# Kernel optimization log

Measured on AMD Instinct MI355X. Metric: run time of the kernel, lower is better.

The kernel has to match this reference:

```python
import jax, jax.numpy as jnp
from jax import lax
import numpy as np

H_SIZE = 1024      # max(hidden_size_list)
EXPAND = 2
INTER = EXPAND * H_SIZE            # 2048 intermediate size
NHEADS = 32                        # max(num_heads_list)
HEAD_DIM = INTER // NHEADS         # 64
NSTATE = 128                       # ssm state size
NGROUPS = 1
KCONV = 4                          # conv kernel
CHUNK = 256                        # chunk size for SSD scan
EPS = 1e-5                         # layer_norm_epsilon
CONV_DIM = INTER + 2 * NGROUPS * NSTATE        # 2304
PROJ_DIM = 2 * INTER + 2 * NGROUPS * NSTATE + NHEADS  # 4352


def setup_inputs() -> dict:
    key = jax.random.key(0)
    ks = jax.random.split(key, 9)
    B, S = 2, 4096
    return {
        "hidden_states": jax.random.normal(ks[0], (B, S, H_SIZE), jnp.float32),
        "in_proj_w": jax.random.normal(ks[1], (PROJ_DIM, H_SIZE), jnp.float32) * 0.02,
        "conv_w": jax.random.normal(ks[2], (CONV_DIM, 1, KCONV), jnp.float32) * 0.2,
        "conv_b": jax.random.normal(ks[3], (CONV_DIM,), jnp.float32) * 0.02,
        "dt_bias": jax.random.normal(ks[4], (NHEADS,), jnp.float32) * 0.1,
        "A_log": jax.random.uniform(ks[5], (NHEADS,), jnp.float32, 0.0, 1.0),
        "D": jax.random.normal(ks[6], (NHEADS,), jnp.float32),
        "norm_w": jnp.ones((INTER,), jnp.float32) + 0.01 * jax.random.normal(ks[7], (INTER,), jnp.float32),
        "out_proj_w": jax.random.normal(ks[8], (H_SIZE, INTER), jnp.float32) * 0.02,
    }


def _segsum(a):
    # a: [B,H,C,L] -> lower-triangular segment sums [B,H,C,L,L]
    L = a.shape[-1]
    cs = jnp.cumsum(a, axis=-1)
    ss = cs[..., :, None] - cs[..., None, :]
    mask = jnp.tril(jnp.ones((L, L), dtype=bool))
    return jnp.where(mask, ss, -jnp.inf)


def reference(hidden_states, in_proj_w, conv_w, conv_b, dt_bias, A_log, D, norm_w, out_proj_w):
    B, S, _ = hidden_states.shape
    proj = hidden_states @ in_proj_w.T                       # [B,S,4352]
    gate = proj[..., :INTER]                                 # [B,S,2048]
    hBC = proj[..., INTER:INTER + CONV_DIM]                  # [B,S,2304]
    dt = proj[..., INTER + CONV_DIM:]                        # [B,S,H]

    # causal depthwise conv1d + SiLU
    xc_ = jnp.transpose(hBC, (0, 2, 1))                      # [B,C,S]
    xc_ = lax.conv_general_dilated(xc_, conv_w, (1,), [(KCONV - 1, 0)],
                                   dimension_numbers=('NCH', 'OIH', 'NCH'),
                                   feature_group_count=CONV_DIM)
    xc_ = jax.nn.silu(xc_ + conv_b[None, :, None])
    hBC = jnp.transpose(xc_, (0, 2, 1))                      # [B,S,2304]

    h = hBC[..., :INTER]
    Bm = hBC[..., INTER:INTER + NGROUPS * NSTATE]
    Cm = hBC[..., INTER + NGROUPS * NSTATE:]

    dt = jax.nn.softplus(dt + dt_bias)                       # [B,S,H]
    dt = jnp.clip(dt, 0.0, None)                             # time_step_limit (0, inf)
    A = -jnp.exp(A_log)                                      # [H]

    NC = S // CHUNK
    xh = h.reshape(B, NC, CHUNK, NHEADS, HEAD_DIM)
    Bh = jnp.repeat(Bm.reshape(B, NC, CHUNK, NGROUPS, NSTATE), NHEADS // NGROUPS, axis=3)
    Ch = jnp.repeat(Cm.reshape(B, NC, CHUNK, NGROUPS, NSTATE), NHEADS // NGROUPS, axis=3)
    dtc = dt.reshape(B, NC, CHUNK, NHEADS)

    a = jnp.transpose(dtc * A, (0, 3, 1, 2))                 # [B,H,NC,L]
    A_cum = jnp.cumsum(a, axis=-1)                           # [B,H,NC,L]
    Lmat = jnp.exp(_segsum(a))                               # [B,H,NC,L,L]
    xdt = xh * dtc[..., None]                                # [B,NC,L,H,P]

    # intra-chunk (diagonal block) output
    Yd = jnp.einsum('bclhn,bcshn,bhcls,bcshp->bclhp', Ch, Bh, Lmat, xdt)

    # per-chunk final states
    decay = jnp.exp(A_cum[..., -1:] - A_cum)                 # [B,H,NC,L]
    states = jnp.einsum('bclhn,bhcl,bclhp->bchpn', Bh, decay, xdt)  # [B,NC,H,P,N]

    # inter-chunk recurrence over chunks
    g = jnp.exp(A_cum[..., -1])                              # [B,H,NC]
    def step(carry, inp):
        s_c, g_c = inp
        return carry * g_c[..., None, None] + s_c, carry
    _, prev = lax.scan(step, jnp.zeros((B, NHEADS, HEAD_DIM, NSTATE), states.dtype),
                       (jnp.moveaxis(states, 1, 0), jnp.moveaxis(g, 2, 0)))
    prev = jnp.moveaxis(prev, 0, 1)                          # [B,NC,H,P,N] state entering each chunk

    Yo = jnp.einsum('bclhn,bchpn,bhcl->bclhp', Ch, prev, jnp.exp(A_cum))

    y = (Yd + Yo + D[None, None, None, :, None] * xh).reshape(B, S, INTER)

    # gated RMSNorm (fp32 internally)
    yf = y.astype(jnp.float32) * jax.nn.silu(gate.astype(jnp.float32))
    var = jnp.mean(yf * yf, axis=-1, keepdims=True)
    y = norm_w * (yf * lax.rsqrt(var + EPS))

    return y @ out_proj_w.T
```

## Files before the change

kernel.cpp:

```cpp
#include <hip/hip_runtime.h>
#include <hip/hip_bf16.h>
#include <math.h>

#define H_SIZE   1024
#define INTER    2048
#define NHEADS   32
#define HEAD_DIM 64
#define NSTATE   128
#define KCONV    4
#define CHUNK    256
#define CONV_DIM (INTER + 2*NSTATE)
#define CIN_DIM  (CONV_DIM + NHEADS)
#define PROJ_DIM (2*INTER + 2*NSTATE + NHEADS)
#define BATCH    2
#define SEQ      4096
#define NC       (SEQ/CHUNK)
#define EPS_F    1e-5f

typedef __attribute__((ext_vector_type(8))) short bf16x8;
typedef __attribute__((ext_vector_type(4))) float f32x4;
typedef unsigned short ushort_t;

__device__ __forceinline__ ushort_t f2bf(float x) {
  unsigned u = __float_as_uint(x);
  u += 0x7fffu + ((u >> 16) & 1u);
  return (ushort_t)(u >> 16);
}
__device__ __forceinline__ float bf2f(ushort_t h) {
  return __uint_as_float((unsigned)h << 16);
}

__global__ __launch_bounds__(256) void convert_hl_kernel(
    const float* __restrict__ x, ushort_t* __restrict__ hi,
    ushort_t* __restrict__ lo, int n4) {
  int idx = blockIdx.x * 256 + threadIdx.x;
  int stride = gridDim.x * 256;
  for (int i = idx; i < n4; i += stride) {
    const float* p = x + (size_t)i * 4;
    float v0 = p[0], v1 = p[1], v2 = p[2], v3 = p[3];
    ushort_t h0 = f2bf(v0), h1 = f2bf(v1), h2 = f2bf(v2), h3 = f2bf(v3);
    ushort_t l0 = f2bf(v0 - bf2f(h0));
    ushort_t l1 = f2bf(v1 - bf2f(h1));
    ushort_t l2 = f2bf(v2 - bf2f(h2));
    ushort_t l3 = f2bf(v3 - bf2f(h3));
    *(uint2*)(hi + (size_t)i * 4) =
        make_uint2((unsigned)h0 | ((unsigned)h1 << 16), (unsigned)h2 | ((unsigned)h3 << 16));
    *(uint2*)(lo + (size_t)i * 4) =
        make_uint2((unsigned)l0 | ((unsigned)l1 << 16), (unsigned)l2 | ((unsigned)l3 << 16));
  }
}

#define LROW 40
template<int PLANES>
__global__ __launch_bounds__(256) void gemm_hl_mfma_kernel(
    const ushort_t* __restrict__ Ahi, const ushort_t* __restrict__ Alo,
    const ushort_t* __restrict__ Whi, const ushort_t* __restrict__ Wlo,
    float* __restrict__ C, int M, int N, int K, int nx, int ldc) {
  __shared__ __align__(16) ushort_t Ah[128*LROW];
  __shared__ __align__(16) ushort_t Al[(PLANES==3) ? 128*LROW : 8];
  __shared__ __align__(16) ushort_t Wh[128*LROW], Wl[128*LROW];
  const int tid = threadIdx.x;
  const int lane = tid & 63, wid = tid >> 6;
  const int wr = wid >> 1, wc = wid & 1;
  const int fr = lane & 15, fg = lane >> 4;

  const int cpx = gridDim.x >> 3;
  const int logical = (blockIdx.x & 7) * cpx + (blockIdx.x >> 3);
  const int grp = logical / (nx * 4);
  const int rem = logical - grp * (nx * 4);
  const int bx = rem >> 2;
  const int by = grp * 4 + (rem & 3);
  const int m0 = by * 128, n0 = bx * 128;

  const int r0 = tid >> 2;
  const int kseg = (tid & 3) * 8;
  const int r1 = r0 + 64;
  const size_t a0 = (size_t)(m0 + r0) * K + kseg;
  const size_t a1 = (size_t)(m0 + r1) * K + kseg;
  const size_t w0 = (size_t)(n0 + r0) * K + kseg;
  const size_t w1 = (size_t)(n0 + r1) * K + kseg;
  const bool wv0 = (n0 + r0) < N, wv1 = (n0 + r1) < N;

  bf16x8 gA0, gA1, gAl0, gAl1, gW0, gW1, gWl0, gWl1;
  const bf16x8 z8 = {};
  f32x4 acc[4][4] = {};

  auto glod = [&](int k0) {
    gA0  = *(const bf16x8*)(Ahi + a0 + k0);
    gA1  = *(const bf16x8*)(Ahi + a1 + k0);
    if constexpr (PLANES == 3) {
      gAl0 = *(const bf16x8*)(Alo + a0 + k0);
      gAl1 = *(const bf16x8*)(Alo + a1 + k0);
    }
    gW0  = wv0 ? *(const bf16x8*)(Whi + w0 + k0) : z8;
    gW1  = wv1 ? *(const bf16x8*)(Whi + w1 + k0) : z8;
    gWl0 = wv0 ? *(const bf16x8*)(Wlo + w0 + k0) : z8;
    gWl1 = wv1 ? *(const bf16x8*)(Wlo + w1 + k0) : z8;
  };

  glod(0);
  for (int k0 = 0; k0 < K; k0 += 32) {
    __syncthreads();
    *(bf16x8*)&Ah[r0*LROW + kseg] = gA0;
    *(bf16x8*)&Ah[r1*LROW + kseg] = gA1;
    if constexpr (PLANES == 3) {
      *(bf16x8*)&Al[r0*LROW + kseg] = gAl0;
      *(bf16x8*)&Al[r1*LROW + kseg] = gAl1;
    }
    *(bf16x8*)&Wh[r0*LROW + kseg] = gW0;
    *(bf16x8*)&Wh[r1*LROW + kseg] = gW1;
    *(bf16x8*)&Wl[r0*LROW + kseg] = gWl0;
    *(bf16x8*)&Wl[r1*LROW + kseg] = gWl1;
    __syncthreads();
    if (k0 + 32 < K) glod(k0 + 32);

    bf16x8 wh[4], wl[4];
#pragma unroll
    for (int nf = 0; nf < 4; ++nf) {
      int off = (wc*64 + nf*16 + fr) * LROW + 8*fg;
      wh[nf] = *(const bf16x8*)&Wh[off];
      wl[nf] = *(const bf16x8*)&Wl[off];
    }
#pragma unroll
    for (int mf = 0; mf < 4; ++mf) {
      int aoff = (wr*64 + mf*16 + fr) * LROW + 8*fg;
      bf16x8 ah = *(const bf16x8*)&Ah[aoff];
      bf16x8 al;
      if constexpr (PLANES == 3) al = *(const bf16x8*)&Al[aoff];
#pragma unroll
      for (int nf = 0; nf < 4; ++nf) {
        acc[mf][nf] = __builtin_amdgcn_mfma_f32_16x16x32_bf16(ah, wh[nf], acc[mf][nf], 0, 0, 0);
        acc[mf][nf] = __builtin_amdgcn_mfma_f32_16x16x32_bf16(ah, wl[nf], acc[mf][nf], 0, 0, 0);
        if constexpr (PLANES == 3)
          acc[mf][nf] = __builtin_amdgcn_mfma_f32_16x16x32_bf16(al, wh[nf], acc[mf][nf], 0, 0, 0);
      }
    }
  }

#pragma unroll
  for (int mf = 0; mf < 4; ++mf)
#pragma unroll
    for (int nf = 0; nf < 4; ++nf) {
      int col = n0 + wc*64 + nf*16 + fr;
      if (col < N) {
        size_t base = (size_t)(m0 + wr*64 + mf*16 + fg*4) * ldc + col;
        f32x4 v = acc[mf][nf];
        C[base]                 = v[0];
        C[base + (size_t)ldc]   = v[1];
        C[base + 2*(size_t)ldc] = v[2];
        C[base + 3*(size_t)ldc] = v[3];
      }
    }
}

__global__ __launch_bounds__(256) void conv2_kernel(
    const float* __restrict__ cin, const float* __restrict__ cw,
    const float* __restrict__ cb, float* __restrict__ hbc,
    ushort_t* __restrict__ Bph, ushort_t* __restrict__ Bpl,
    ushort_t* __restrict__ Cph, ushort_t* __restrict__ Cpl) {
  const int c = blockIdx.x * 256 + threadIdx.x;
  const int r0 = blockIdx.y * 8;
  const int s0 = r0 & (SEQ - 1);
  const float w0 = cw[c*KCONV+0], w1 = cw[c*KCONV+1];
  const float w2 = cw[c*KCONV+2], w3 = cw[c*KCONV+3];
  const float bias = cb[c];
  const float* cp = cin + (size_t)r0 * CIN_DIM + c;
  float xm3 = (s0 > 0) ? cp[-3*CIN_DIM] : 0.f;
  float xm2 = (s0 > 0) ? cp[-2*CIN_DIM] : 0.f;
  float xm1 = (s0 > 0) ? cp[-1*CIN_DIM] : 0.f;
#pragma unroll
  for (int i = 0; i < 8; ++i) {
    float x0 = cp[(size_t)i * CIN_DIM];
    float acc = fmaf(w0, xm3, fmaf(w1, xm2, fmaf(w2, xm1, fmaf(w3, x0, bias))));
    acc = acc / (1.f + expf(-acc));
    size_t row = (size_t)(r0 + i);
    if (c < INTER) {
      hbc[row*CONV_DIM + c] = acc;
    } else {
      ushort_t hh = f2bf(acc);
      ushort_t ll = f2bf(acc - bf2f(hh));
      int cc = c - INTER;
      if (cc < NSTATE) { Bph[row*NSTATE + cc] = hh; Bpl[row*NSTATE + cc] = ll; }
      else { Cph[row*NSTATE + (cc-NSTATE)] = hh; Cpl[row*NSTATE + (cc-NSTATE)] = ll; }
    }
    xm3 = xm2; xm2 = xm1; xm1 = x0;
  }
}

__global__ __launch_bounds__(256) void cumsum_kernel(
    const float* __restrict__ cin, const float* __restrict__ A_log,
    const float* __restrict__ dtb, float* __restrict__ dtp,
    float* __restrict__ acum, float* __restrict__ gch) {
  const int c = blockIdx.x, h = blockIdx.y, b = blockIdx.z;
  const int tid = threadIdx.x;
  __shared__ float sm[CHUNK];
  const float A = -expf(A_log[h]);
  const int s = c * CHUNK + tid;
  const size_t row = (size_t)(b*SEQ + s);
  float draw = cin[row*CIN_DIM + CONV_DIM + h] + dtb[h];
  float d = (draw > 20.f) ? draw : log1pf(expf(draw));
  dtp[row*NHEADS + h] = d;
  float a = d * A;
  sm[tid] = a;
  __syncthreads();
  for (int off = 1; off < CHUNK; off <<= 1) {
    float v = 0.f;
    if (tid >= off) v = sm[tid - off];
    __syncthreads();
    sm[tid] += v;
    __syncthreads();
  }
  float ac = sm[tid];
  acum[((size_t)(b*NHEADS + h)*NC + c)*CHUNK + tid] = ac;
  if (tid == CHUNK-1) gch[(size_t)(b*NHEADS + h)*NC + c] = expf(ac);
}

#define CBROW 136
#define XROW2 72
__global__ __launch_bounds__(256) void yd_mfma_kernel(
    const ushort_t* __restrict__ Bph, const ushort_t* __restrict__ Bpl,
    const ushort_t* __restrict__ Cph, const ushort_t* __restrict__ Cpl,
    const float* __restrict__ hbc, const float* __restrict__ acum,
    const float* __restrict__ dtp, const float* __restrict__ Dv,
    float* __restrict__ y) {
  __shared__ __align__(16) ushort_t BhS[64*CBROW], BlS[64*CBROW];
  __shared__ __align__(16) ushort_t XhS[64*XROW2], XlS[64*XROW2];
  __shared__ __align__(16) ushort_t GhS[4][16*XROW2], GlS[4][16*XROW2];
  __shared__ float acLs[64], acSs[64];

  const int h = blockIdx.x;
  const int c = blockIdx.y >> 2, lt = blockIdx.y & 3;
  const int b = blockIdx.z;
  const int tid = threadIdx.x;
  const int lane = tid & 63, w = tid >> 6;
  const int fr = lane & 15, fg = lane >> 4;

  const size_t seqbase = (size_t)(b*SEQ + c*CHUNK);
  const size_t acbase  = ((size_t)(b*NHEADS + h)*NC + c)*CHUNK;

  bf16x8 cfh[4], cfl[4];
  {
    const size_t cg = (seqbase + lt*64 + w*16 + fr) * 128;
#pragma unroll
    for (int ks = 0; ks < 4; ++ks) {
      int ko = ks*32 + fg*8;
      cfh[ks] = *(const bf16x8*)(Cph + cg + ko);
      cfl[ks] = *(const bf16x8*)(Cpl + cg + ko);
    }
  }
  if (tid < 64) acLs[tid] = acum[acbase + lt*64 + tid];

  f32x4 acc[4] = {};

  for (int st = 0; st <= lt; ++st) {
    __syncthreads();
    {
      const size_t g0 = (seqbase + st*64) * 128;
#pragma unroll
      for (int i = 0; i < 4; ++i) {
        int f = tid + 256*i; int r = f >> 4; int k8 = (f & 15) * 8;
        *(bf16x8*)&BhS[r*CBROW + k8] = *(const bf16x8*)(Bph + g0 + (size_t)r*128 + k8);
        *(bf16x8*)&BlS[r*CBROW + k8] = *(const bf16x8*)(Bpl + g0 + (size_t)r*128 + k8);
      }
    }
#pragma unroll
    for (int i = 0; i < 4; ++i) {
      int f = tid + 256*i; int s = f >> 4; int p0 = (f & 15) * 4;
      size_t row = seqbase + st*64 + s;
      float dtv = dtp[row*NHEADS + h];
      float4 xv = *(const float4*)(hbc + row*CONV_DIM + h*HEAD_DIM + p0);
      float vals[4] = {xv.x*dtv, xv.y*dtv, xv.z*dtv, xv.w*dtv};
#pragma unroll
      for (int j = 0; j < 4; ++j) {
        int p = p0 + j;
        int sw = s ^ (((p >> 2) & 7) << 3);
        ushort_t hh = f2bf(vals[j]);
        ushort_t ll = f2bf(vals[j] - bf2f(hh));
        XhS[p*XROW2 + sw] = hh;
        XlS[p*XROW2 + sw] = ll;
      }
    }
    if (tid < 64) acSs[tid] = acum[acbase + st*64 + tid];
    __syncthreads();

    f32x4 g[4] = {};
#pragma unroll
    for (int ks = 0; ks < 4; ++ks) {
      const int ko = ks*32 + fg*8;
#pragma unroll
      for (int nf = 0; nf < 4; ++nf) {
        const int rb = (nf*16 + fr) * CBROW + ko;
        bf16x8 bh = *(const bf16x8*)&BhS[rb];
        bf16x8 bl = *(const bf16x8*)&BlS[rb];
        g[nf] = __builtin_amdgcn_mfma_f32_16x16x32_bf16(cfh[ks], bh, g[nf], 0, 0, 0);
        g[nf] = __builtin_amdgcn_mfma_f32_16x16x32_bf16(cfh[ks], bl, g[nf], 0, 0, 0);
        g[nf] = __builtin_amdgcn_mfma_f32_16x16x32_bf16(cfl[ks], bh, g[nf], 0, 0, 0);
      }
    }
    {
      const bool full = (st < lt);
#pragma unroll
      for (int nf = 0; nf < 4; ++nf) {
        int sl = nf*16 + fr;
        float aS = acSs[sl];
#pragma unroll
        for (int r = 0; r < 4; ++r) {
          int ll = w*16 + fg*4 + r;
          float v = 0.f;
          if (full || ll >= sl) v = g[nf][r] * __expf(acLs[ll] - aS);
          ushort_t hh = f2bf(v);
          ushort_t lo2 = f2bf(v - bf2f(hh));
          GhS[w][(fg*4 + r)*XROW2 + sl] = hh;
          GlS[w][(fg*4 + r)*XROW2 + sl] = lo2;
        }
      }
    }
    __syncthreads();
#pragma unroll
    for (int ks = 0; ks < 2; ++ks) {
      const int ko = ks*32 + fg*8;
      bf16x8 gh = *(const bf16x8*)&GhS[w][fr*XROW2 + ko];
      bf16x8 gl = *(const bf16x8*)&GlS[w][fr*XROW2 + ko];
#pragma unroll
      for (int nf = 0; nf < 4; ++nf) {
        int p = nf*16 + fr;
        int kb = ko ^ (((p >> 2) & 7) << 3);
        bf16x8 xh = *(const bf16x8*)&XhS[p*XROW2 + kb];
        bf16x8 xl = *(const bf16x8*)&XlS[p*XROW2 + kb];
        acc[nf] = __builtin_amdgcn_mfma_f32_16x16x32_bf16(gh, xh, acc[nf], 0, 0, 0);
        acc[nf] = __builtin_amdgcn_mfma_f32_16x16x32_bf16(gh, xl, acc[nf], 0, 0, 0);
        acc[nf] = __builtin_amdgcn_mfma_f32_16x16x32_bf16(gl, xh, acc[nf], 0, 0, 0);
      }
    }
  }

  const float Dh = Dv[h];
#pragma unroll
  for (int nf = 0; nf < 4; ++nf) {
    int p = nf*16 + fr;
#pragma unroll
    for (int r = 0; r < 4; ++r) {
      size_t row = seqbase + lt*64 + w*16 + fg*4 + r;
      float xval = hbc[row*CONV_DIM + h*HEAD_DIM + p];
      y[row*INTER + h*HEAD_DIM + p] = acc[nf][r] + Dh * xval;
    }
  }
}

#define SXROW 72
__global__ __launch_bounds__(256) void states_mfma_kernel(
    const ushort_t* __restrict__ Bph, const ushort_t* __restrict__ Bpl,
    const float* __restrict__ hbc, const float* __restrict__ acum,
    const float* __restrict__ dtp, float* __restrict__ states) {
  __shared__ __align__(16) ushort_t XhS[64*SXROW], XlS[64*SXROW];
  __shared__ __align__(16) ushort_t BhS[128*SXROW], BlS[128*SXROW];
  const int h = blockIdx.x, c = blockIdx.y, b = blockIdx.z;
  const int tid = threadIdx.x;
  const int lane = tid & 63, w = tid >> 6;
  const int fr = lane & 15, fg = lane >> 4;
  const size_t seqbase = (size_t)(b*SEQ + c*CHUNK);
  const size_t acbase  = ((size_t)(b*NHEADS + h)*NC + c)*CHUNK;
  const float aclast = acum[acbase + CHUNK - 1];
  f32x4 acc[8] = {};

  for (int lt = 0; lt < 4; ++lt) {
    __syncthreads();
#pragma unroll
    for (int i = 0; i < 4; ++i) {
      int f = tid + 256*i; int l = f >> 4; int p0 = (f & 15) * 4;
      size_t row = seqbase + lt*64 + l;
      float mult = dtp[row*NHEADS + h] * __expf(aclast - acum[acbase + lt*64 + l]);
      float4 xv = *(const float4*)(hbc + row*CONV_DIM + h*HEAD_DIM + p0);
      float vals[4] = {xv.x*mult, xv.y*mult, xv.z*mult, xv.w*mult};
#pragma unroll
      for (int j = 0; j < 4; ++j) {
        int p = p0 + j;
        int sw = l ^ (((p >> 2) & 7) << 3);
        ushort_t hh = f2bf(vals[j]);
        XhS[p*SXROW + sw] = hh;
        XlS[p*SXROW + sw] = f2bf(vals[j] - bf2f(hh));
      }
    }
#pragma unroll
    for (int i = 0; i < 4; ++i) {
      int f = tid + 256*i; int l = f >> 4; int n8 = (f & 15) * 8;
      size_t g0 = (seqbase + lt*64 + l) * 128 + n8;
      bf16x8 bh = *(const bf16x8*)(Bph + g0);
      bf16x8 bl = *(const bf16x8*)(Bpl + g0);
#pragma unroll
      for (int j = 0; j < 8; ++j) {
        int n = n8 + j;
        int sw = l ^ (((n >> 2) & 7) << 3);
        BhS[n*SXROW + sw] = (ushort_t)bh[j];
        BlS[n*SXROW + sw] = (ushort_t)bl[j];
      }
    }
    __syncthreads();
#pragma unroll
    for (int ks = 0; ks < 2; ++ks) {
      const int ko = ks*32 + fg*8;
      const int pa = w*16 + fr;
      const int ka = ko ^ (((pa >> 2) & 7) << 3);
      bf16x8 ah = *(const bf16x8*)&XhS[pa*SXROW + ka];
      bf16x8 al = *(const bf16x8*)&XlS[pa*SXROW + ka];
#pragma unroll
      for (int nf = 0; nf < 8; ++nf) {
        const int nb = nf*16 + fr;
        const int kb = ko ^ (((nb >> 2) & 7) << 3);
        bf16x8 bh = *(const bf16x8*)&BhS[nb*SXROW + kb];
        bf16x8 bl = *(const bf16x8*)&BlS[nb*SXROW + kb];
        acc[nf] = __builtin_amdgcn_mfma_f32_16x16x32_bf16(ah, bh, acc[nf], 0, 0, 0);
        acc[nf] = __builtin_amdgcn_mfma_f32_16x16x32_bf16(ah, bl, acc[nf], 0, 0, 0);
        acc[nf] = __builtin_amdgcn_mfma_f32_16x16x32_bf16(al, bh, acc[nf], 0, 0, 0);
      }
    }
  }
  float* sp = states + ((size_t)(b*NC + c)*NHEADS + h)*HEAD_DIM*NSTATE;
#pragma unroll
  for (int nf = 0; nf < 8; ++nf) {
    int n = nf*16 + fr;
#pragma unroll
    for (int r = 0; r < 4; ++r) {
      int p = w*16 + fg*4 + r;
      sp[(size_t)p*NSTATE + n] = acc[nf][r];
    }
  }
}

__global__ __launch_bounds__(1024) void scan_kernel(
    float* __restrict__ st, const float* __restrict__ g) {
  const int bh = blockIdx.x;
  const int b = bh >> 5, h = bh & 31;
  const int tid = threadIdx.x;
  float carry[8];
#pragma unroll
  for (int i = 0; i < 8; ++i) carry[i] = 0.f;
  for (int c = 0; c < NC; ++c) {
    const float gc = g[(size_t)(b*NHEADS + h)*NC + c];
    float* base = st + ((size_t)(b*NC + c)*NHEADS + h)*HEAD_DIM*NSTATE;
    ushort_t* ub = (ushort_t*)base;
    float sv[8];
#pragma unroll
    for (int i = 0; i < 8; ++i) sv[i] = base[i*1024 + tid];
    __syncthreads();
#pragma unroll
    for (int i = 0; i < 8; ++i) {
      int e = i*1024 + tid;
      ushort_t hh = f2bf(carry[i]);
      ub[e]        = hh;
      ub[8192 + e] = f2bf(carry[i] - bf2f(hh));
      carry[i] = fmaf(carry[i], gc, sv[i]);
    }
  }
}

#define PROW 136
__global__ __launch_bounds__(256) void yo_mfma_kernel(
    const ushort_t* __restrict__ Cph, const ushort_t* __restrict__ Cpl,
    const ushort_t* __restrict__ stp, const float* __restrict__ acum,
    float* __restrict__ y) {
  __shared__ __align__(16) ushort_t PhS[64*PROW], PlS[64*PROW];
  const int h = blockIdx.x, c = blockIdx.y, b = blockIdx.z;
  const int tid = threadIdx.x;
  const int lane = tid & 63, w = tid >> 6;
  const int fr = lane & 15, fg = lane >> 4;
  const size_t seqbase = (size_t)(b*SEQ + c*CHUNK);
  const size_t acbase  = ((size_t)(b*NHEADS + h)*NC + c)*CHUNK;

  const ushort_t* pb = stp + ((size_t)(b*NC + c)*NHEADS + h) * (size_t)(2*HEAD_DIM*NSTATE);
#pragma unroll
  for (int i = 0; i < 4; ++i) {
    int f = tid + 256*i; int r = f >> 4; int k8 = (f & 15) * 8;
    *(bf16x8*)&PhS[r*PROW + k8] = *(const bf16x8*)(pb + (size_t)r*128 + k8);
    *(bf16x8*)&PlS[r*PROW + k8] = *(const bf16x8*)(pb + 8192 + (size_t)r*128 + k8);
  }
  __syncthreads();

  for (int lt = 0; lt < 4; ++lt) {
    const size_t cg = (seqbase + lt*64 + w*16 + fr) * 128;
    f32x4 acc[4] = {};
#pragma unroll
    for (int ks = 0; ks < 4; ++ks) {
      int ko = ks*32 + fg*8;
      bf16x8 ah = *(const bf16x8*)(Cph + cg + ko);
      bf16x8 al = *(const bf16x8*)(Cpl + cg + ko);
#pragma unroll
      for (int nf = 0; nf < 4; ++nf) {
        const int rb = (nf*16 + fr) * PROW + ko;
        bf16x8 bh = *(const bf16x8*)&PhS[rb];
        bf16x8 bl = *(const bf16x8*)&PlS[rb];
        acc[nf] = __builtin_amdgcn_mfma_f32_16x16x32_bf16(ah, bh, acc[nf], 0, 0, 0);
        acc[nf] = __builtin_amdgcn_mfma_f32_16x16x32_bf16(ah, bl, acc[nf], 0, 0, 0);
        acc[nf] = __builtin_amdgcn_mfma_f32_16x16x32_bf16(al, bh, acc[nf], 0, 0, 0);
      }
    }
#pragma unroll
    for (int r = 0; r < 4; ++r) {
      int lrow = lt*64 + w*16 + fg*4 + r;
      float e = __expf(acum[acbase + lrow]);
      float* yrow = y + (seqbase + lrow)*INTER + h*HEAD_DIM;
#pragma unroll
      for (int nf = 0; nf < 4; ++nf) {
        int p = nf*16 + fr;
        yrow[p] += e * acc[nf][r];
      }
    }
  }
}

__global__ __launch_bounds__(256) void rms_kernel(
    const float* __restrict__ y, const float* __restrict__ gate,
    const float* __restrict__ norm_w, ushort_t* __restrict__ yh) {
  const int bs = blockIdx.x;
  const int tid = threadIdx.x;
  const float* yrow = y + (size_t)bs * INTER;
  const float* grow = gate + (size_t)bs * INTER;
  float yf[8];
  float ss = 0.f;
#pragma unroll
  for (int i = 0; i < 8; ++i) {
    int c = tid + i*256;
    float v = yrow[c];
    float gt = grow[c];
    float f = v * (gt / (1.f + expf(-gt)));
    yf[i] = f;
    ss += f*f;
  }
#pragma unroll
  for (int off = 32; off >= 1; off >>= 1) ss += __shfl_xor(ss, off, 64);
  __shared__ float red[4];
  if ((tid & 63) == 0) red[tid >> 6] = ss;
  __syncthreads();
  float total = red[0] + red[1] + red[2] + red[3];
  float sc = rsqrtf(total * (1.f/INTER) + EPS_F);
#pragma unroll
  for (int i = 0; i < 8; ++i) {
    int c = tid + i*256;
    yh[(size_t)bs*INTER + c] = f2bf(norm_w[c] * yf[i] * sc);
  }
}

__global__ void zero_kernel(float* p, size_t n) {
  size_t i = (size_t)blockIdx.x * blockDim.x + threadIdx.x;
  if (i < n) p[i] = 0.f;
}

extern "C" void kernel_launch(void* const* d_in, const int* in_sizes, int n_in,
                              void* d_out, int out_size, void* d_ws, size_t ws_size,
                              hipStream_t stream) {
  const float* hidden = (const float*)d_in[0];
  const float* in_w   = (const float*)d_in[1];
  const float* conv_w = (const float*)d_in[2];
  const float* conv_b = (const float*)d_in[3];
  const float* dt_b   = (const float*)d_in[4];
  const float* A_log  = (const float*)d_in[5];
  const float* Dv     = (const float*)d_in[6];
  const float* norm_w = (const float*)d_in[7];
  const float* out_w  = (const float*)d_in[8];
  float* out = (float*)d_out;

  const int M = BATCH*SEQ;

  const size_t sz_cin  = (size_t)M * CIN_DIM;
  const size_t sz_hbc  = (size_t)M * CONV_DIM;
  const size_t sz_dtp  = (size_t)M * NHEADS;
  const size_t sz_acum = (size_t)BATCH*NHEADS*NC*CHUNK;
  const size_t sz_gch  = (size_t)BATCH*NHEADS*NC;
  const size_t sz_R    = (size_t)BATCH*NC*NHEADS*HEAD_DIM*NSTATE;
  const size_t need = (sz_cin + sz_hbc + sz_dtp + sz_acum + sz_gch + sz_R) * sizeof(float);

  if (ws_size < need) {
    size_t n = (size_t)out_size;
    zero_kernel<<<(unsigned)((n + 255) / 256), 256, 0, stream>>>(out, n);
    return;
  }

  float* ws = (float*)d_ws;
  size_t o = 0;
  float* cin  = ws + o; o += sz_cin;
  float* hbc  = ws + o; o += sz_hbc;
  float* dtp  = ws + o; o += sz_dtp;
  float* acum = ws + o; o += sz_acum;
  float* gch  = ws + o; o += sz_gch;
  float* R    = ws + o; o += sz_R;

  float* y    = cin;
  float* gate = hbc;
  float* st   = R;

  ushort_t* hidhi = (ushort_t*)R;
  ushort_t* hidlo = hidhi + (size_t)M * H_SIZE;
  ushort_t* yhR   = (ushort_t*)R;
  ushort_t* wplh  = (ushort_t*)hbc;

  ushort_t* wscr = (ushort_t*)out;
  const size_t MP = (size_t)M * 128;
  ushort_t* bcp  = (ushort_t*)((char*)d_out + (size_t)(16u << 20));
  ushort_t* Bph = bcp;
  ushort_t* Bpl = bcp + MP;
  ushort_t* Cph = bcp + 2*MP;
  ushort_t* Cpl = bcp + 3*MP;

  {
    int nA4 = (M * H_SIZE) / 4;
    int nW  = CIN_DIM * H_SIZE;
    convert_hl_kernel<<<2048, 256, 0, stream>>>(hidden, hidhi, hidlo, nA4);
    convert_hl_kernel<<<2048, 256, 0, stream>>>(in_w + (size_t)INTER*H_SIZE, wscr, wscr + nW, nW/4);
    gemm_hl_mfma_kernel<2><<<16 * (M/128), 256, 0, stream>>>(
        hidhi, hidlo, wscr, wscr + nW, cin, M, 2048, H_SIZE, 16, CIN_DIM);
    gemm_hl_mfma_kernel<3><<<3 * (M/128), 256, 0, stream>>>(
        hidhi, hidlo, wscr + (size_t)2048*H_SIZE, wscr + nW + (size_t)2048*H_SIZE,
        cin + 2048, M, 288, H_SIZE, 3, CIN_DIM);
  }
  conv2_kernel<<<dim3(CONV_DIM/256, M/8), 256, 0, stream>>>(
      cin, conv_w, conv_b, hbc, Bph, Bpl, Cph, Cpl);
  cumsum_kernel<<<dim3(NC, NHEADS, BATCH), 256, 0, stream>>>(
      cin, A_log, dt_b, dtp, acum, gch);
  yd_mfma_kernel<<<dim3(NHEADS, NC*4, BATCH), 256, 0, stream>>>(
      Bph, Bpl, Cph, Cpl, hbc, acum, dtp, Dv, y);
  states_mfma_kernel<<<dim3(NHEADS, NC, BATCH), 256, 0, stream>>>(
      Bph, Bpl, hbc, acum, dtp, st);
  scan_kernel<<<dim3(BATCH*NHEADS), 1024, 0, stream>>>(st, gch);
  yo_mfma_kernel<<<dim3(NHEADS, NC, BATCH), 256, 0, stream>>>(
      Cph, Cpl, (const ushort_t*)st, acum, y);
  {
    int nA4 = (M * H_SIZE) / 4;
    int nW  = INTER * H_SIZE;
    convert_hl_kernel<<<2048, 256, 0, stream>>>(hidden, hidhi, hidlo, nA4);
    convert_hl_kernel<<<2048, 256, 0, stream>>>(in_w, wscr, wscr + nW, nW/4);
    gemm_hl_mfma_kernel<2><<<16 * (M/128), 256, 0, stream>>>(
        hidhi, hidlo, wscr, wscr + nW, gate, M, INTER, H_SIZE, 16, INTER);
  }
  rms_kernel<<<dim3(M), 256, 0, stream>>>(y, gate, norm_w, yhR);
  {
    int nW  = H_SIZE * INTER;
    convert_hl_kernel<<<2048, 256, 0, stream>>>(out_w, wplh, wplh + nW, nW/4);
    gemm_hl_mfma_kernel<2><<<8 * (M/128), 256, 0, stream>>>(
        yhR, yhR, wplh, wplh + nW, out, M, H_SIZE, INTER, 8, H_SIZE);
  }
}
```

Baseline: 659.6 us.

## Store conv output transposed as bf16 hi/lo pairs, read directly in MFMA kernels

```diff
diff --git a/kernel.cpp b/kernel.cpp
--- a/kernel.cpp
+++ b/kernel.cpp
@@ -11,9 +11,9 @@
 #define CHUNK    256
 #define CONV_DIM (INTER + 2*NSTATE)
 #define CIN_DIM  (CONV_DIM + NHEADS)
-#define PROJ_DIM (2*INTER + 2*NSTATE + NHEADS)
 #define BATCH    2
 #define SEQ      4096
+#define MT       (BATCH*SEQ)
 #define NC       (SEQ/CHUNK)
 #define EPS_F    1e-5f
 
@@ -155,11 +155,12 @@
 
 __global__ __launch_bounds__(256) void conv2_kernel(
     const float* __restrict__ cin, const float* __restrict__ cw,
-    const float* __restrict__ cb, float* __restrict__ hbc,
-    ushort_t* __restrict__ Bph, ushort_t* __restrict__ Bpl,
-    ushort_t* __restrict__ Cph, ushort_t* __restrict__ Cpl) {
+    const float* __restrict__ cb, ushort_t* __restrict__ xTh,
+    ushort_t* __restrict__ xTl, ushort_t* __restrict__ Bph,
+    ushort_t* __restrict__ Bpl, ushort_t* __restrict__ Cph,
+    ushort_t* __restrict__ Cpl) {
   const int c = blockIdx.x * 256 + threadIdx.x;
-  const int r0 = blockIdx.y * 8;
+  const int r0 = blockIdx.y * 32;
   const int s0 = r0 & (SEQ - 1);
   const float w0 = cw[c*KCONV+0], w1 = cw[c*KCONV+1];
   const float w2 = cw[c*KCONV+2], w3 = cw[c*KCONV+3];
@@ -168,22 +169,42 @@
   float xm3 = (s0 > 0) ? cp[-3*CIN_DIM] : 0.f;
   float xm2 = (s0 > 0) ? cp[-2*CIN_DIM] : 0.f;
   float xm1 = (s0 > 0) ? cp[-1*CIN_DIM] : 0.f;
-#pragma unroll
-  for (int i = 0; i < 8; ++i) {
-    float x0 = cp[(size_t)i * CIN_DIM];
-    float acc = fmaf(w0, xm3, fmaf(w1, xm2, fmaf(w2, xm1, fmaf(w3, x0, bias))));
-    acc = acc / (1.f + expf(-acc));
-    size_t row = (size_t)(r0 + i);
-    if (c < INTER) {
-      hbc[row*CONV_DIM + c] = acc;
-    } else {
+
+  if (c < INTER) {
+    ushort_t hb[32], lb[32];
+#pragma unroll
+    for (int i = 0; i < 32; ++i) {
+      float x0 = cp[(size_t)i * CIN_DIM];
+      float acc = fmaf(w0, xm3, fmaf(w1, xm2, fmaf(w2, xm1, fmaf(w3, x0, bias))));
+      acc = acc / (1.f + expf(-acc));
+      ushort_t hh = f2bf(acc);
+      hb[i] = hh; lb[i] = f2bf(acc - bf2f(hh));
+      xm3 = xm2; xm2 = xm1; xm1 = x0;
+    }
+    ushort_t* ph = xTh + (size_t)c * MT + r0;
+    ushort_t* pl = xTl + (size_t)c * MT + r0;
+#pragma unroll
+    for (int j = 0; j < 4; ++j) {
+      bf16x8 vh, vl;
+#pragma unroll
+      for (int k = 0; k < 8; ++k) { vh[k] = (short)hb[j*8+k]; vl[k] = (short)lb[j*8+k]; }
+      *(bf16x8*)(ph + j*8) = vh;
+      *(bf16x8*)(pl + j*8) = vl;
+    }
+  } else {
+    const int cc = c - INTER;
+#pragma unroll
+    for (int i = 0; i < 32; ++i) {
+      float x0 = cp[(size_t)i * CIN_DIM];
+      float acc = fmaf(w0, xm3, fmaf(w1, xm2, fmaf(w2, xm1, fmaf(w3, x0, bias))));
+      acc = acc / (1.f + expf(-acc));
+      size_t row = (size_t)(r0 + i);
       ushort_t hh = f2bf(acc);
       ushort_t ll = f2bf(acc - bf2f(hh));
-      int cc = c - INTER;
       if (cc < NSTATE) { Bph[row*NSTATE + cc] = hh; Bpl[row*NSTATE + cc] = ll; }
       else { Cph[row*NSTATE + (cc-NSTATE)] = hh; Cpl[row*NSTATE + (cc-NSTATE)] = ll; }
-    }
-    xm3 = xm2; xm2 = xm1; xm1 = x0;
+      xm3 = xm2; xm2 = xm1; xm1 = x0;
+    }
   }
 }
 
@@ -216,17 +237,16 @@
 }
 
 #define CBROW 136
-#define XROW2 72
+#define GROW  72
 __global__ __launch_bounds__(256) void yd_mfma_kernel(
     const ushort_t* __restrict__ Bph, const ushort_t* __restrict__ Bpl,
     const ushort_t* __restrict__ Cph, const ushort_t* __restrict__ Cpl,
-    const float* __restrict__ hbc, const float* __restrict__ acum,
-    const float* __restrict__ dtp, const float* __restrict__ Dv,
-    float* __restrict__ y) {
+    const ushort_t* __restrict__ xTh, const ushort_t* __restrict__ xTl,
+    const float* __restrict__ acum, const float* __restrict__ dtp,
+    const float* __restrict__ Dv, float* __restrict__ y) {
   __shared__ __align__(16) ushort_t BhS[64*CBROW], BlS[64*CBROW];
-  __shared__ __align__(16) ushort_t XhS[64*XROW2], XlS[64*XROW2];
-  __shared__ __align__(16) ushort_t GhS[4][16*XROW2], GlS[4][16*XROW2];
-  __shared__ float acLs[64], acSs[64];
+  __shared__ __align__(16) ushort_t GhS[4][16*GROW], GlS[4][16*GROW];
+  __shared__ float acLs[64], acSs[64], dtSs[64];
 
   const int h = blockIdx.x;
   const int c = blockIdx.y >> 2, lt = blockIdx.y & 3;
@@ -263,24 +283,8 @@
         *(bf16x8*)&BlS[r*CBROW + k8] = *(const bf16x8*)(Bpl + g0 + (size_t)r*128 + k8);
       }
     }
-#pragma unroll
-    for (int i = 0; i < 4; ++i) {
-      int f = tid + 256*i; int s = f >> 4; int p0 = (f & 15) * 4;
-      size_t row = seqbase + st*64 + s;
-      float dtv = dtp[row*NHEADS + h];
-      float4 xv = *(const float4*)(hbc + row*CONV_DIM + h*HEAD_DIM + p0);
-      float vals[4] = {xv.x*dtv, xv.y*dtv, xv.z*dtv, xv.w*dtv};
-#pragma unroll
-      for (int j = 0; j < 4; ++j) {
-        int p = p0 + j;
-        int sw = s ^ (((p >> 2) & 7) << 3);
-        ushort_t hh = f2bf(vals[j]);
-        ushort_t ll = f2bf(vals[j] - bf2f(hh));
-        XhS[p*XROW2 + sw] = hh;
-        XlS[p*XROW2 + sw] = ll;
-      }
-    }
     if (tid < 64) acSs[tid] = acum[acbase + st*64 + tid];
+    else if (tid < 128) dtSs[tid-64] = dtp[(seqbase + st*64 + (tid-64))*NHEADS + h];
     __syncthreads();
 
     f32x4 g[4] = {};
@@ -303,15 +307,16 @@
       for (int nf = 0; nf < 4; ++nf) {
         int sl = nf*16 + fr;
         float aS = acSs[sl];
+        float dS = dtSs[sl];
 #pragma unroll
         for (int r = 0; r < 4; ++r) {
           int ll = w*16 + fg*4 + r;
           float v = 0.f;
-          if (full || ll >= sl) v = g[nf][r] * __expf(acLs[ll] - aS);
+          if (full || ll >= sl) v = g[nf][r] * __expf(acLs[ll] - aS) * dS;
           ushort_t hh = f2bf(v);
           ushort_t lo2 = f2bf(v - bf2f(hh));
-          GhS[w][(fg*4 + r)*XROW2 + sl] = hh;
-          GlS[w][(fg*4 + r)*XROW2 + sl] = lo2;
+          GhS[w][(fg*4 + r)*GROW + sl] = hh;
+          GlS[w][(fg*4 + r)*GROW + sl] = lo2;
         }
       }
     }
@@ -319,14 +324,13 @@
 #pragma unroll
     for (int ks = 0; ks < 2; ++ks) {
       const int ko = ks*32 + fg*8;
-      bf16x8 gh = *(const bf16x8*)&GhS[w][fr*XROW2 + ko];
-      bf16x8 gl = *(const bf16x8*)&GlS[w][fr*XROW2 + ko];
+      bf16x8 gh = *(const bf16x8*)&GhS[w][fr*GROW + ko];
+      bf16x8 gl = *(const bf16x8*)&GlS[w][fr*GROW + ko];
 #pragma unroll
       for (int nf = 0; nf < 4; ++nf) {
-        int p = nf*16 + fr;
-        int kb = ko ^ (((p >> 2) & 7) << 3);
-        bf16x8 xh = *(const bf16x8*)&XhS[p*XROW2 + kb];
-        bf16x8 xl = *(const bf16x8*)&XlS[p*XROW2 + kb];
+        const size_t xb = (size_t)(h*HEAD_DIM + nf*16 + fr) * MT + seqbase + st*64 + ko;
+        bf16x8 xh = *(const bf16x8*)(xTh + xb);
+        bf16x8 xl = *(const bf16x8*)(xTl + xb);
         acc[nf] = __builtin_amdgcn_mfma_f32_16x16x32_bf16(gh, xh, acc[nf], 0, 0, 0);
         acc[nf] = __builtin_amdgcn_mfma_f32_16x16x32_bf16(gh, xl, acc[nf], 0, 0, 0);
         acc[nf] = __builtin_amdgcn_mfma_f32_16x16x32_bf16(gl, xh, acc[nf], 0, 0, 0);
@@ -338,10 +342,11 @@
 #pragma unroll
   for (int nf = 0; nf < 4; ++nf) {
     int p = nf*16 + fr;
+    const size_t xrow0 = (size_t)(h*HEAD_DIM + p) * MT + seqbase + lt*64 + w*16 + fg*4;
 #pragma unroll
     for (int r = 0; r < 4; ++r) {
       size_t row = seqbase + lt*64 + w*16 + fg*4 + r;
-      float xval = hbc[row*CONV_DIM + h*HEAD_DIM + p];
+      float xval = bf2f(xTh[xrow0 + r]) + bf2f(xTl[xrow0 + r]);
       y[row*INTER + h*HEAD_DIM + p] = acc[nf][r] + Dh * xval;
     }
   }
@@ -350,9 +355,9 @@
 #define SXROW 72
 __global__ __launch_bounds__(256) void states_mfma_kernel(
     const ushort_t* __restrict__ Bph, const ushort_t* __restrict__ Bpl,
-    const float* __restrict__ hbc, const float* __restrict__ acum,
-    const float* __restrict__ dtp, float* __restrict__ states) {
-  __shared__ __align__(16) ushort_t XhS[64*SXROW], XlS[64*SXROW];
+    const ushort_t* __restrict__ xTh, const ushort_t* __restrict__ xTl,
+    const float* __restrict__ acum, const float* __restrict__ dtp,
+    float* __restrict__ states) {
   __shared__ __align__(16) ushort_t BhS[128*SXROW], BlS[128*SXROW];
   const int h = blockIdx.x, c = blockIdx.y, b = blockIdx.z;
   const int tid = threadIdx.x;
@@ -367,42 +372,29 @@
     __syncthreads();
 #pragma unroll
     for (int i = 0; i < 4; ++i) {
-      int f = tid + 256*i; int l = f >> 4; int p0 = (f & 15) * 4;
+      int f = tid + 256*i; int l = f >> 4; int n8 = (f & 15) * 8;
       size_t row = seqbase + lt*64 + l;
       float mult = dtp[row*NHEADS + h] * __expf(aclast - acum[acbase + lt*64 + l]);
-      float4 xv = *(const float4*)(hbc + row*CONV_DIM + h*HEAD_DIM + p0);
-      float vals[4] = {xv.x*mult, xv.y*mult, xv.z*mult, xv.w*mult};
-#pragma unroll
-      for (int j = 0; j < 4; ++j) {
-        int p = p0 + j;
-        int sw = l ^ (((p >> 2) & 7) << 3);
-        ushort_t hh = f2bf(vals[j]);
-        XhS[p*SXROW + sw] = hh;
-        XlS[p*SXROW + sw] = f2bf(vals[j] - bf2f(hh));
-      }
-    }
-#pragma unroll
-    for (int i = 0; i < 4; ++i) {
-      int f = tid + 256*i; int l = f >> 4; int n8 = (f & 15) * 8;
-      size_t g0 = (seqbase + lt*64 + l) * 128 + n8;
+      size_t g0 = row * 128 + n8;
       bf16x8 bh = *(const bf16x8*)(Bph + g0);
       bf16x8 bl = *(const bf16x8*)(Bpl + g0);
 #pragma unroll
       for (int j = 0; j < 8; ++j) {
         int n = n8 + j;
         int sw = l ^ (((n >> 2) & 7) << 3);
-        BhS[n*SXROW + sw] = (ushort_t)bh[j];
-        BlS[n*SXROW + sw] = (ushort_t)bl[j];
+        float bv = (bf2f((ushort_t)bh[j]) + bf2f((ushort_t)bl[j])) * mult;
+        ushort_t hh = f2bf(bv);
+        BhS[n*SXROW + sw] = hh;
+        BlS[n*SXROW + sw] = f2bf(bv - bf2f(hh));
       }
     }
     __syncthreads();
 #pragma unroll
     for (int ks = 0; ks < 2; ++ks) {
       const int ko = ks*32 + fg*8;
-      const int pa = w*16 + fr;
-      const int ka = ko ^ (((pa >> 2) & 7) << 3);
-      bf16x8 ah = *(const bf16x8*)&XhS[pa*SXROW + ka];
-      bf16x8 al = *(const bf16x8*)&XlS[pa*SXROW + ka];
+      const size_t xb = (size_t)(h*HEAD_DIM + w*16 + fr) * MT + seqbase + lt*64 + ko;
+      bf16x8 ah = *(const bf16x8*)(xTh + xb);
+      bf16x8 al = *(const bf16x8*)(xTl + xb);
 #pragma unroll
       for (int nf = 0; nf < 8; ++nf) {
         const int nb = nf*16 + fr;
@@ -559,7 +551,7 @@
   const float* out_w  = (const float*)d_in[8];
   float* out = (float*)d_out;
 
-  const int M = BATCH*SEQ;
+  const int M = MT;
 
   const size_t sz_cin  = (size_t)M * CIN_DIM;
   const size_t sz_hbc  = (size_t)M * CONV_DIM;
@@ -587,6 +579,9 @@
   float* y    = cin;
   float* gate = hbc;
   float* st   = R;
+
+  ushort_t* xTh = (ushort_t*)hbc;
+  ushort_t* xTl = xTh + (size_t)INTER * MT;
 
   ushort_t* hidhi = (ushort_t*)R;
   ushort_t* hidlo = hidhi + (size_t)M * H_SIZE;
@@ -612,14 +607,14 @@
         hidhi, hidlo, wscr + (size_t)2048*H_SIZE, wscr + nW + (size_t)2048*H_SIZE,
         cin + 2048, M, 288, H_SIZE, 3, CIN_DIM);
   }
-  conv2_kernel<<<dim3(CONV_DIM/256, M/8), 256, 0, stream>>>(
-      cin, conv_w, conv_b, hbc, Bph, Bpl, Cph, Cpl);
+  conv2_kernel<<<dim3(CONV_DIM/256, M/32), 256, 0, stream>>>(
+      cin, conv_w, conv_b, xTh, xTl, Bph, Bpl, Cph, Cpl);
   cumsum_kernel<<<dim3(NC, NHEADS, BATCH), 256, 0, stream>>>(
       cin, A_log, dt_b, dtp, acum, gch);
   yd_mfma_kernel<<<dim3(NHEADS, NC*4, BATCH), 256, 0, stream>>>(
-      Bph, Bpl, Cph, Cpl, hbc, acum, dtp, Dv, y);
+      Bph, Bpl, Cph, Cpl, xTh, xTl, acum, dtp, Dv, y);
   states_mfma_kernel<<<dim3(NHEADS, NC, BATCH), 256, 0, stream>>>(
-      Bph, Bpl, hbc, acum, dtp, st);
+      Bph, Bpl, xTh, xTl, acum, dtp, st);
   scan_kernel<<<dim3(BATCH*NHEADS), 1024, 0, stream>>>(st, gch);
   yo_mfma_kernel<<<dim3(NHEADS, NC, BATCH), 256, 0, stream>>>(
       Cph, Cpl, (const ushort_t*)st, acum, y);
```

New measurement: 748.5 us. 1.13x slower.
